# Optimization experiments

Measured on AMD Instinct MI355X. Metric: run time of the kernel, lower is better.

Reference implementation:

```python
import jax, jax.numpy as jnp
import numpy as np
import math

B, L, C_IN = 64, 3168, 64
D_MODEL, K = 512, 16  # K = cycle_length (kernel width == stride)
W = L // K            # 198 output tokens from deform conv


def _positional(S, d, dtype):
    # PositionalEmbedding buffer, rows [0, S)
    pos = jnp.arange(S, dtype=jnp.float32)[:, None]
    div = jnp.exp(jnp.arange(0, d, 2, dtype=jnp.float32) * (-math.log(10000.0) / d))
    pe = jnp.zeros((S, d), jnp.float32)
    pe = pe.at[:, 0::2].set(jnp.sin(pos * div))
    pe = pe.at[:, 1::2].set(jnp.cos(pos * div))
    return pe.astype(dtype)


def setup_inputs() -> dict:
    key = jax.random.key(0)
    ks = jax.random.split(key, 6)
    fan_in = C_IN * K
    std = math.sqrt(2.0 / (1 + 0.01 ** 2) / fan_in)  # kaiming_normal, leaky_relu fan_in
    return {
        "x": jax.random.normal(ks[0], (B, L, C_IN), jnp.float32),
        "w_off": jax.random.normal(ks[1], (2 * K, C_IN, K), jnp.float32) * std,
        "b_off": jax.random.normal(ks[2], (2 * K,), jnp.float32) * 0.02,
        "w_def": jax.random.normal(ks[3], (D_MODEL, C_IN, K), jnp.float32) * std,
        "b_def": jax.random.normal(ks[4], (D_MODEL,), jnp.float32) * 0.02,
        "cls_token": jax.random.normal(ks[5], (1, 1, D_MODEL), jnp.float32),
    }


def _gather_cols(xt, idx, L_):
    # xt: (B, C, L); idx: (B, K, W) int32 -> (B, C, K, W), zero out-of-bounds
    b, c = xt.shape[0], xt.shape[1]
    valid = (idx >= 0) & (idx < L_)
    idxc = jnp.clip(idx, 0, L_ - 1).reshape(b, 1, -1)
    g = jnp.take_along_axis(xt, jnp.broadcast_to(idxc, (b, c, idxc.shape[-1])), axis=2)
    g = g.reshape(b, c, idx.shape[1], idx.shape[2])
    return jnp.where(valid[:, None], g, 0.0)


def reference(x, w_off, b_off, w_def, b_def, cls_token):
    b, l, c = x.shape
    w = l // K
    # offset conv: kernel (1,K), stride (1,K) == non-overlapping windows
    xr = x[:, : w * K, :].reshape(b, w, K, c)              # (B, W, K, C)
    off = jnp.einsum('bwkc,ock->bow', xr, w_off) + b_off[None, :, None]  # (B, 2K, W)
    dy = off[:, 0::2]                                      # (B, K, W)
    dx = off[:, 1::2]
    # sampling positions along width (height is size 1, base y = 0)
    base = (jnp.arange(w)[None, :] * K + jnp.arange(K)[:, None]).astype(x.dtype)  # (K, W)
    px = base[None] + dx                                   # (B, K, W)
    x0 = jnp.floor(px)
    frac = px - x0
    x0i = x0.astype(jnp.int32)
    xt = x.transpose(0, 2, 1)                              # (B, C, L)
    v0 = _gather_cols(xt, x0i, l)
    v1 = _gather_cols(xt, x0i + 1, l)
    wy = jnp.maximum(0.0, 1.0 - jnp.abs(dy))               # vertical bilinear weight on row 0
    val = wy[:, None] * ((1.0 - frac)[:, None] * v0 + frac[:, None] * v1)  # (B, C, K, W)
    out = jnp.einsum('bckw,dck->bwd', val, w_def) + b_def  # (B, W, d_model)
    tok = jnp.concatenate([jnp.broadcast_to(cls_token, (b, 1, D_MODEL)), out], axis=1)
    pe = _positional(w + 1, D_MODEL, tok.dtype)
    return tok + pe[None]
```

## Files before the change

### kernel.cpp

```cpp
#include <hip/hip_runtime.h>
#include <math.h>
#include <stdint.h>

#define NB 64
#define NL 3168
#define NC 64
#define ND 512
#define NK 16
#define NW 198
#define NM 12672
#define KD 1024

typedef __attribute__((ext_vector_type(8))) short bf8_t;
typedef __attribute__((ext_vector_type(4))) float f4_t;

typedef const unsigned int __attribute__((address_space(1)))* as1_u32p;
typedef unsigned int __attribute__((address_space(3)))* as3_u32p;

__device__ __forceinline__ void gl_lds16(const void* g, void* l) {
  __builtin_amdgcn_global_load_lds((as1_u32p)(uintptr_t)g,
                                   (as3_u32p)(unsigned int)(uintptr_t)l, 16, 0, 0);
}

__device__ __forceinline__ unsigned short f2bf(float f) {
  union { float f; unsigned u; } v; v.f = f;
  unsigned r = v.u + 0x7FFFu + ((v.u >> 16) & 1u);
  return (unsigned short)(r >> 16);
}

__global__ void prep_kernel(const float* __restrict__ w_off, const float* __restrict__ w_def,
                            const float* __restrict__ cls, unsigned short* __restrict__ wofft,
                            unsigned short* __restrict__ wdeft, float* __restrict__ pe,
                            float* __restrict__ out) {
  int id = blockIdx.x * 256 + threadIdx.x;
  if (id < 131072) {
    float4 v = ((const float4*)w_def)[id];
    ushort4 o;
    o.x = f2bf(v.x); o.y = f2bf(v.y); o.z = f2bf(v.z); o.w = f2bf(v.w);
    ((ushort4*)wdeft)[id] = o;
    return;
  }
  id -= 131072;
  if (id < 32768) {
    int o = id >> 10, kc = id & 1023, k = kc >> 6, c = kc & 63;
    wofft[id] = f2bf(w_off[o * 1024 + c * 16 + k]);
    return;
  }
  id -= 32768;
  if (id < 101888) {
    int pos = id >> 9, d = id & 511;
    int i = d >> 1;
    float freq = expf((float)(2 * i) * (-9.210340371976184f / 512.0f));
    float arg = (float)pos * freq;
    pe[id] = (d & 1) ? cosf(arg) : sinf(arg);
    return;
  }
  id -= 101888;
  {
    int b = id >> 9, d = id & 511;
    out[(size_t)(b * 199) * 512 + d] = cls[d] + ((d & 1) ? 1.0f : 0.0f);
  }
}

__launch_bounds__(512)
__global__ void offsample_kernel(const float* __restrict__ x,
                                 const unsigned short* __restrict__ wofft,
                                 const float* __restrict__ b_off,
                                 unsigned short* __restrict__ val_ws) {
  __shared__ float partial[8][16][33];
  __shared__ float2 s_w[16][16];
  __shared__ int2   s_i[16][16];
  __shared__ int    s_base[16];
  int tid = threadIdx.x;
  int lane = tid & 63, wid = tid >> 6;
  int r16 = lane & 15, kg = lane >> 4;
  int flat = blockIdx.x;
  int bsw = (flat & 7) * 99 + (flat >> 3);
  int row0 = bsw * 16;

  f4_t acc[2] = {};
  const float* arow = x + (size_t)(row0 + r16) * KD + wid * 128;
  const unsigned short* bcol0 = wofft + r16 * KD + wid * 128;
  const unsigned short* bcol1 = wofft + (16 + r16) * KD + wid * 128;

#pragma unroll
  for (int ks = 0; ks < 4; ++ks) {
    int k0 = ks * 32 + kg * 8;
    float4 v0 = *(const float4*)(arow + k0);
    float4 v1 = *(const float4*)(arow + k0 + 4);
    bf8_t a;
    a[0] = (short)f2bf(v0.x); a[1] = (short)f2bf(v0.y);
    a[2] = (short)f2bf(v0.z); a[3] = (short)f2bf(v0.w);
    a[4] = (short)f2bf(v1.x); a[5] = (short)f2bf(v1.y);
    a[6] = (short)f2bf(v1.z); a[7] = (short)f2bf(v1.w);
    bf8_t b0 = *(const bf8_t*)(bcol0 + k0);
    bf8_t b1 = *(const bf8_t*)(bcol1 + k0);
    acc[0] = __builtin_amdgcn_mfma_f32_16x16x32_bf16(a, b0, acc[0], 0, 0, 0);
    acc[1] = __builtin_amdgcn_mfma_f32_16x16x32_bf16(a, b1, acc[1], 0, 0, 0);
  }
#pragma unroll
  for (int n = 0; n < 2; ++n)
#pragma unroll
    for (int r = 0; r < 4; ++r)
      partial[wid][kg * 4 + r][n * 16 + r16] = acc[n][r];
  __syncthreads();

  if (tid < 256) {
    int rp = tid >> 4, k = tid & 15;
    float dy = b_off[2 * k], dx = b_off[2 * k + 1];
#pragma unroll
    for (int w8 = 0; w8 < 8; ++w8) {
      dy += partial[w8][rp][2 * k];
      dx += partial[w8][rp][2 * k + 1];
    }
    int rg = row0 + rp;
    int b = rg / NW, w = rg - b * NW;
    if (k == 0) s_base[rp] = b * (NL * NC);
    float wy = fmaxf(0.f, 1.f - fabsf(dy));
    float px = (float)(w * 16 + k) + dx;
    float x0f = floorf(px);
    float frac = px - x0f;
    int x0 = (int)x0f;
    float w0 = wy * (1.f - frac), w1 = wy * frac;
    if (x0 < 0 || x0 >= NL) w0 = 0.f;
    if (x0 + 1 < 0 || x0 + 1 >= NL) w1 = 0.f;
    int x0c = min(max(x0, 0), NL - 1);
    int x1c = min(max(x0 + 1, 0), NL - 1);
    s_w[rp][k] = make_float2(w0, w1);
    s_i[rp][k] = make_int2(x0c * 64, x1c * 64);
  }
  __syncthreads();

#pragma unroll
  for (int rr = 0; rr < 2; ++rr) {
    int rp = wid * 2 + rr;
    const float* xb = x + s_base[rp];
    unsigned short vv[16];
#pragma unroll
    for (int k = 0; k < 16; ++k) {
      float2 wk = s_w[rp][k];
      int2 ik = s_i[rp][k];
      float v0 = xb[ik.x + lane];
      float v1 = xb[ik.y + lane];
      vv[k] = f2bf(wk.x * v0 + wk.y * v1);
    }
    unsigned int p[8];
#pragma unroll
    for (int i = 0; i < 8; ++i)
      p[i] = (unsigned int)vv[2 * i] | ((unsigned int)vv[2 * i + 1] << 16);
    int rg = row0 + rp;
    uint4* dst = (uint4*)(val_ws + (size_t)rg * KD + lane * 16);
    dst[0] = make_uint4(p[0], p[1], p[2], p[3]);
    dst[1] = make_uint4(p[4], p[5], p[6], p[7]);
  }
}

__launch_bounds__(128)
__global__ void gemm_kernel(const unsigned short* __restrict__ val_ws,
                            const unsigned short* __restrict__ wdeft,
                            const float* __restrict__ b_def, const float* __restrict__ pe,
                            float* __restrict__ out) {
  __shared__ unsigned short As[2][128 * 64];
  __shared__ unsigned short Bs[2][64 * 64];
  int tid = threadIdx.x;
  int flat = blockIdx.x;
  int w = (flat & 7) * 99 + (flat >> 3);
  int mt = w >> 3, nt = w & 7;
  int lane = tid & 63, wid = tid >> 6;
  int r16 = lane & 15, kg = lane >> 4;
  f4_t acc[4][4] = {};

  int r_st = lane >> 3;
  int j_st = lane & 7;
  const char* aBase = (const char*)val_ws + (size_t)mt * 128 * 2048;
  const char* bBase = (const char*)wdeft + (size_t)nt * 64 * 2048;

  auto STAGE = [&](int ks, int buf) {
#pragma unroll
    for (int i = 0; i < 8; ++i) {
      int seg = wid * 8 + i;
      int r = seg * 8 + r_st;
      int src_off = ((j_st ^ (r & 7)) << 4);
      gl_lds16(aBase + (size_t)r * 2048 + ks * 128 + src_off, &As[buf][seg * 512]);
    }
#pragma unroll
    for (int i = 0; i < 4; ++i) {
      int seg = wid * 4 + i;
      int r = seg * 8 + r_st;
      int src_off = ((j_st ^ (r & 7)) << 4);
      gl_lds16(bBase + (size_t)r * 2048 + ks * 128 + src_off, &Bs[buf][seg * 512]);
    }
  };

  auto COMPUTE = [&](int buf) {
#pragma unroll
    for (int jb = 0; jb < 8; jb += 4) {
      bf8_t af[4], bf[4];
#pragma unroll
      for (int m = 0; m < 4; ++m) {
        int R = wid * 64 + m * 16 + r16;
        af[m] = *(const bf8_t*)&As[buf][R * 64 + (((jb + kg) ^ (R & 7)) << 3)];
      }
#pragma unroll
      for (int n = 0; n < 4; ++n) {
        int Rc = n * 16 + r16;
        bf[n] = *(const bf8_t*)&Bs[buf][Rc * 64 + (((jb + kg) ^ (Rc & 7)) << 3)];
      }
#pragma unroll
      for (int m = 0; m < 4; ++m)
#pragma unroll
        for (int n = 0; n < 4; ++n)
          acc[m][n] = __builtin_amdgcn_mfma_f32_16x16x32_bf16(af[m], bf[n], acc[m][n], 0, 0, 0);
    }
  };

  STAGE(0, 0);
  asm volatile("s_waitcnt vmcnt(0)" ::: "memory");
  __builtin_amdgcn_s_barrier();
#pragma unroll
  for (int t = 0; t < 16; ++t) {
    if (t < 15) {
      STAGE(t + 1, (t + 1) & 1);
      asm volatile("s_waitcnt vmcnt(12)" ::: "memory");
    } else {
      asm volatile("s_waitcnt vmcnt(0)" ::: "memory");
    }
    __builtin_amdgcn_s_barrier();
    COMPUTE(t & 1);
    asm volatile("s_waitcnt lgkmcnt(0)" ::: "memory");
    __builtin_amdgcn_sched_barrier(0);
    __builtin_amdgcn_s_barrier();
  }

#pragma unroll
  for (int m = 0; m < 4; ++m)
#pragma unroll
    for (int n = 0; n < 4; ++n)
#pragma unroll
      for (int r = 0; r < 4; ++r) {
        int grow = mt * 128 + wid * 64 + m * 16 + kg * 4 + r;
        int gcol = nt * 64 + n * 16 + r16;
        int bi = grow / NW, wi = grow - bi * NW;
        out[((size_t)(bi * 199 + wi + 1)) * 512 + gcol] =
            acc[m][n][r] + b_def[gcol] + pe[(wi + 1) * 512 + gcol];
      }
}

extern "C" void kernel_launch(void* const* d_in, const int* in_sizes, int n_in,
                              void* d_out, int out_size, void* d_ws, size_t ws_size,
                              hipStream_t stream) {
  const float* x     = (const float*)d_in[0];
  const float* w_off = (const float*)d_in[1];
  const float* b_off = (const float*)d_in[2];
  const float* w_def = (const float*)d_in[3];
  const float* b_def = (const float*)d_in[4];
  const float* cls   = (const float*)d_in[5];
  float* out = (float*)d_out;
  char* ws = (char*)d_ws;
  unsigned short* val_ws = (unsigned short*)ws;
  unsigned short* wofft  = (unsigned short*)(ws + 25952256);
  unsigned short* wdeft  = (unsigned short*)(ws + 26017792);
  float* pe              = (float*)(ws + 27066368);

  prep_kernel<<<1166, 256, 0, stream>>>(w_off, w_def, cls, wofft, wdeft, pe, out);
  offsample_kernel<<<NM / 16, 512, 0, stream>>>(x, wofft, b_off, val_ws);
  gemm_kernel<<<792, 128, 0, stream>>>(val_ws, wdeft, b_def, pe, out);
}
```

Before: 61.39 us.

## Reorder GEMM K layout to (c/4,k,c%4) for vectorized gather loads

Changes the flattened K dimension of the sampled-value workspace and the bf16 deform weights from (c,k) to (c/4, k, c%4) ordering. The gather kernel can then load float4 of four channels per sample position and store ushort4, instead of doing scalar per-channel loads. Both producer layouts are changed consistently, so the GEMM contraction stays correct. The weight prep now does scattered 2-byte stores, and the gather's output stores become less contiguous per lane.

```diff
diff --git a/kernel.cpp b/kernel.cpp
--- a/kernel.cpp
+++ b/kernel.cpp
@@ -35,9 +35,10 @@
   int id = blockIdx.x * 256 + threadIdx.x;
   if (id < 131072) {
     float4 v = ((const float4*)w_def)[id];
-    ushort4 o;
-    o.x = f2bf(v.x); o.y = f2bf(v.y); o.z = f2bf(v.z); o.w = f2bf(v.w);
-    ((ushort4*)wdeft)[id] = o;
+    int e = id * 4;
+    int d = e >> 10, c = (e >> 4) & 63, k0 = e & 15;
+    unsigned short* dst = wdeft + d * 1024 + (c >> 2) * 64 + k0 * 4 + (c & 3);
+    dst[0] = f2bf(v.x); dst[4] = f2bf(v.y); dst[8] = f2bf(v.z); dst[12] = f2bf(v.w);
     return;
   }
   id -= 131072;
@@ -131,27 +132,26 @@
   }
   __syncthreads();
 
+  int c4 = lane >> 2, kq = lane & 3;
 #pragma unroll
   for (int rr = 0; rr < 2; ++rr) {
     int rp = wid * 2 + rr;
     const float* xb = x + s_base[rp];
-    unsigned short vv[16];
-#pragma unroll
-    for (int k = 0; k < 16; ++k) {
+    unsigned short* rowdst = val_ws + (size_t)(row0 + rp) * KD;
+#pragma unroll
+    for (int p = 0; p < 4; ++p) {
+      int k = p * 4 + kq;
       float2 wk = s_w[rp][k];
       int2 ik = s_i[rp][k];
-      float v0 = xb[ik.x + lane];
-      float v1 = xb[ik.y + lane];
-      vv[k] = f2bf(wk.x * v0 + wk.y * v1);
-    }
-    unsigned int p[8];
-#pragma unroll
-    for (int i = 0; i < 8; ++i)
-      p[i] = (unsigned int)vv[2 * i] | ((unsigned int)vv[2 * i + 1] << 16);
-    int rg = row0 + rp;
-    uint4* dst = (uint4*)(val_ws + (size_t)rg * KD + lane * 16);
-    dst[0] = make_uint4(p[0], p[1], p[2], p[3]);
-    dst[1] = make_uint4(p[4], p[5], p[6], p[7]);
+      float4 v0 = *(const float4*)(xb + ik.x + c4 * 4);
+      float4 v1 = *(const float4*)(xb + ik.y + c4 * 4);
+      ushort4 o;
+      o.x = f2bf(wk.x * v0.x + wk.y * v1.x);
+      o.y = f2bf(wk.x * v0.y + wk.y * v1.y);
+      o.z = f2bf(wk.x * v0.z + wk.y * v1.z);
+      o.w = f2bf(wk.x * v0.w + wk.y * v1.w);
+      *(ushort4*)(rowdst + c4 * 64 + k * 4) = o;
+    }
   }
 }
 
```

After: 67.27 us. 1.1x slower.
